# Performance work log

Measured on AMD Instinct MI355X. Metric: run time of the kernel, lower is better.

## Reference

```python
import jax, jax.numpy as jnp
import numpy as np

JACCARD_THRESH = 0.5
NEG_POS = 3
VAR0, VAR1 = 0.1, 0.2
MAX_POS = 256  # static cap on gathered positives for the metric-learning terms


def point_form(boxes):
    # (cx,cy,w,h) -> (xmin,ymin,xmax,ymax)
    return jnp.concatenate([boxes[:, :2] - boxes[:, 2:] / 2,
                            boxes[:, :2] + boxes[:, 2:] / 2], axis=1)


def jaccard(a, b):
    # a: [O,4], b: [D,4] point form
    lt = jnp.maximum(a[:, None, :2], b[None, :, :2])
    rb = jnp.minimum(a[:, None, 2:], b[None, :, 2:])
    wh = jnp.clip(rb - lt, 0.0)
    inter = wh[..., 0] * wh[..., 1]
    area_a = (a[:, 2] - a[:, 0]) * (a[:, 3] - a[:, 1])
    area_b = (b[:, 2] - b[:, 0]) * (b[:, 3] - b[:, 1])
    return inter / (area_a[:, None] + area_b[None, :] - inter)


def encode(matched, priors):
    g_cxcy = ((matched[:, :2] + matched[:, 2:]) / 2 - priors[:, :2]) / (VAR0 * priors[:, 2:])
    g_wh = jnp.log((matched[:, 2:] - matched[:, :2]) / priors[:, 2:]) / VAR1
    return jnp.concatenate([g_cxcy, g_wh], axis=1)


def match_one(truths, labels, poses, priors):
    # standard SSD match (per image)
    ov = jaccard(truths, point_form(priors))          # [O, D]
    best_prior_idx = jnp.argmax(ov, axis=1)           # [O]
    best_truth_ov = jnp.max(ov, axis=0)               # [D]
    best_truth_idx = jnp.argmax(ov, axis=0)           # [D]
    best_truth_ov = best_truth_ov.at[best_prior_idx].set(2.0)
    best_truth_idx = best_truth_idx.at[best_prior_idx].set(jnp.arange(truths.shape[0]))
    matches = truths[best_truth_idx]                  # [D,4]
    conf = labels[best_truth_idx] + 1                 # background=0
    conf = jnp.where(best_truth_ov < JACCARD_THRESH, 0, conf)
    return encode(matches, priors), conf.astype(jnp.int32), poses[best_truth_idx]


def multibox_loss(loc_data, conf_data, line_data, pose_data, dbox_list, targets):
    B, D, C = conf_data.shape
    truths = targets[:, :, 0:4]
    labels = targets[:, :, 4].astype(jnp.int32)
    poses = targets[:, :, 5:8]
    loc_t, conf_t, pose_t = jax.vmap(match_one, in_axes=(0, 0, 0, None))(
        truths, labels, poses, dbox_list)

    pos = conf_t > 0                                  # [B,D]
    posf = pos.astype(loc_data.dtype)

    # smooth-L1 loc loss over positives (sum reduction)
    d = loc_data - loc_t
    sl1 = jnp.where(jnp.abs(d) < 1.0, 0.5 * d * d, jnp.abs(d) - 0.5)
    loss_l = jnp.sum(sl1 * posf[..., None])

    # pose squared-error over positives
    loss_p = jnp.sum((pose_data - pose_t) ** 2 * posf[..., None])

    # per-anchor cross entropy + hard-negative mining (double-argsort rank trick)
    logp = jax.nn.log_softmax(conf_data, axis=-1)
    ce = -jnp.take_along_axis(logp, conf_t[..., None], axis=-1)[..., 0]  # [B,D]
    ce_mined = jnp.where(pos, 0.0, ce)
    loss_idx = jnp.argsort(-ce_mined, axis=1)
    idx_rank = jnp.argsort(loss_idx, axis=1)
    num_pos = jnp.sum(pos.astype(jnp.int32), axis=1, keepdims=True)
    num_neg = jnp.minimum(num_pos * NEG_POS, D)
    neg = idx_rank < num_neg
    loss_c = jnp.sum(ce * (pos | neg).astype(ce.dtype))

    N = jnp.maximum(jnp.sum(posf), 1.0)
    loss_l = loss_l / N
    loss_c = loss_c / N
    loss_p = loss_p / N

    # ---- metric-learning block on gathered positives (static cap) ----
    pos_flat = pos.reshape(-1)
    order = jnp.argsort(jnp.where(pos_flat, 0, 1))[:MAX_POS]  # stable: row-major positives first
    valid = pos_flat[order]                                   # [K]
    emb = line_data.reshape(-1, line_data.shape[-1])[order]   # [K,32] raw embeddings
    lab = conf_t.reshape(-1)[order]                           # [K]
    qp = pose_t.reshape(-1, 3)[order]                         # [K,3]

    # PairMarginMiner / TripletMarginLoss use L2-normalized LpDistance by default
    nemb = emb / jnp.maximum(jnp.linalg.norm(emb, axis=1, keepdims=True), 1e-12)
    sq = jnp.sum((nemb[:, None, :] - nemb[None, :, :]) ** 2, axis=-1)
    dist = jnp.sqrt(jnp.maximum(sq, 1e-12))                   # [K,K]

    K = emb.shape[0]
    eye = jnp.eye(K, dtype=bool)
    vpair = valid[:, None] & valid[None, :] & ~eye
    same = lab[:, None] == lab[None, :]
    pos_pair = vpair & same & (dist > 0.2)   # mined hard positive pairs
    neg_pair = vpair & ~same & (dist < 0.8)  # mined hard negative pairs
    n_pp = jnp.sum(pos_pair)
    n_np = jnp.sum(neg_pair)

    # pairs -> triplets sharing the anchor; TripletMarginLoss(margin=0.2), AvgNonZero reducer
    trip_mask = pos_pair[:, :, None] & neg_pair[:, None, :]           # [K,K,K]
    trip_loss = jax.nn.relu(dist[:, :, None] - dist[:, None, :] + 0.2)
    nz = trip_mask & (trip_loss > 0)
    loss_t = jnp.sum(jnp.where(nz, trip_loss, 0.0)) / jnp.maximum(jnp.sum(nz), 1)

    # Ldesk over mined positive pairs: raw-embedding sq-dist vs pose sq-dist consistency
    e_sq = jnp.sum((emb[:, None, :] - emb[None, :, :]) ** 2, axis=-1)
    q_sq = jnp.sum((qp[:, None, :] - qp[None, :, :]) ** 2, axis=-1)
    desk_sum = jnp.sum(jnp.where(pos_pair, (e_sq - q_sq) ** 2, 0.0))
    npp = jnp.maximum(n_pp, 1).astype(loc_data.dtype)
    Ldesk = desk_sum / npp + loss_t / jnp.maximum(n_pp + n_np, 1)
    Ldesk = Ldesk / npp / 32.0

    return loss_l, loss_c, loss_p, Ldesk, loss_t


def setup_inputs():
    key = jax.random.key(0)
    ks = jax.random.split(key, 10)
    B, D, C, L, O = 32, 8732, 21, 32, 8
    loc_data = jax.random.normal(ks[0], (B, D, 4)) * 0.1
    conf_data = jax.random.normal(ks[1], (B, D, C))
    line_data = jax.random.normal(ks[2], (B, D, L))
    pose_data = jax.random.normal(ks[3], (B, D, 3))
    # default boxes (cx,cy,w,h) in (0,1)
    cxcy = jax.random.uniform(ks[4], (D, 2), minval=0.05, maxval=0.95)
    wh = jax.random.uniform(ks[5], (D, 2), minval=0.05, maxval=0.4)
    dbox_list = jnp.concatenate([cxcy, wh], axis=1)
    # targets: [xmin,ymin,xmax,ymax,label,pose(3),unused]
    mins = jax.random.uniform(ks[6], (B, O, 2), minval=0.0, maxval=0.6)
    sizes = jax.random.uniform(ks[7], (B, O, 2), minval=0.1, maxval=0.4)
    boxes = jnp.concatenate([mins, mins + sizes], axis=-1)
    labs = jax.random.randint(ks[8], (B, O, 1), 0, C - 1).astype(jnp.float32)
    pz = jax.random.normal(ks[9], (B, O, 3))
    targets = jnp.concatenate([boxes, labs, pz, jnp.zeros((B, O, 1))], axis=-1)
    return dict(loc_data=loc_data, conf_data=conf_data, line_data=line_data,
                pose_data=pose_data, dbox_list=dbox_list, targets=targets)


def reference(loc_data, conf_data, line_data, pose_data, dbox_list, targets):
    return multibox_loss(loc_data, conf_data, line_data, pose_data, dbox_list, targets)
```

## Files before the change

kernel.cpp:

```cpp
#include <hip/hip_runtime.h>
#include <cstdint>

#define B 32
#define D 8732
#define C 21
#define L 32
#define O 8
#define NSEGB 16
#define SEGLEN 546
#define NSEG 512
#define MT 576
#define NT 1024
#define PAIRB 128
#define TOPB 32
#define FINTGT (PAIRB + TOPB)

struct Ws {
  const float *loc, *conf, *line, *pose, *dbox, *targets;
  float* out;
  unsigned long long* bpPart;
  double* acc;
  int* ictr;
  int* cnt;
  int* posSlice;
  float* sce;
};

__device__ inline double waveSumD(double v) {
  #pragma unroll
  for (int s = 32; s > 0; s >>= 1) v += __shfl_down(v, s, 64);
  return v;
}

__device__ inline float iou_one(float tx1, float ty1, float tx2, float ty2, float ta,
                                float px1, float py1, float px2, float py2, float areaB) {
  float lx = fmaxf(tx1, px1), ly = fmaxf(ty1, py1);
  float rx = fminf(tx2, px2), ry = fminf(ty2, py2);
  float iw = fmaxf(rx - lx, 0.f), ih = fmaxf(ry - ly, 0.f);
  float inter = iw * ih;
  return inter / (ta + areaB - inter);
}

__global__ __launch_bounds__(256) void k_bp(Ws p) {
  __shared__ float tb[O][4], ta[O];
  __shared__ unsigned long long wm[4][O];
  int g = blockIdx.x, tid = threadIdx.x;
  int lane = tid & 63, wav = tid >> 6;
  int b = g >> 4, s = g & 15;
  int dBeg = s * SEGLEN;
  int dEnd = dBeg + SEGLEN; if (dEnd > D) dEnd = D;
  if (g == 0) {
    if (tid < 9) p.acc[tid] = 0.0;
    if (tid == 9) { p.ictr[0] = 0; p.ictr[1] = 0; }
  }
  if (tid < O) {
    const float* tr = p.targets + ((size_t)b * O + tid) * 9;
    tb[tid][0] = tr[0]; tb[tid][1] = tr[1]; tb[tid][2] = tr[2]; tb[tid][3] = tr[3];
    ta[tid] = (tr[2] - tr[0]) * (tr[3] - tr[1]);
  }
  __syncthreads();
  float bi_[O]; int bd_[O];
  #pragma unroll
  for (int t = 0; t < O; t++) { bi_[t] = 0.f; bd_[t] = 0; }
  for (int d = dBeg + tid; d < dEnd; d += 256) {
    float4 db = *(const float4*)(p.dbox + (size_t)d * 4);
    float px1 = db.x - 0.5f*db.z, py1 = db.y - 0.5f*db.w;
    float px2 = db.x + 0.5f*db.z, py2 = db.y + 0.5f*db.w;
    float areaB = db.z * db.w;
    #pragma unroll
    for (int t = 0; t < O; t++) {
      float iou = iou_one(tb[t][0], tb[t][1], tb[t][2], tb[t][3], ta[t],
                          px1, py1, px2, py2, areaB);
      if (iou > bi_[t]) { bi_[t] = iou; bd_[t] = d; }
    }
  }
  #pragma unroll
  for (int t = 0; t < O; t++) {
    unsigned long long k = ((unsigned long long)__float_as_uint(bi_[t]) << 32)
                         | (unsigned long long)(0xFFFFFFFFu - (unsigned)bd_[t]);
    #pragma unroll
    for (int sft = 32; sft > 0; sft >>= 1) {
      unsigned long long o = __shfl_down(k, sft, 64);
      if (o > k) k = o;
    }
    if (lane == 0) wm[wav][t] = k;
  }
  __syncthreads();
  if (tid < O) {
    unsigned long long k = wm[0][tid];
    #pragma unroll
    for (int w = 1; w < 4; w++) if (wm[w][tid] > k) k = wm[w][tid];
    p.bpPart[(size_t)g * O + tid] = k;
  }
}

struct ShM {
  float confS[SEGLEN * C];
  float tb[O][4], ta[O], tl[O], tp_[O][3];
  unsigned long long bpred[128];
  int bpd[O];
  int plist[256];
  int wcnt[9], wbase[9];
  double wred[9][3];
  int run;
};

__global__ __launch_bounds__(MT, 2) void k_match(Ws p) {
  __shared__ ShM sh;
  int g = blockIdx.x, tid = threadIdx.x;
  int lane = tid & 63, wav = tid >> 6;
  int b = g >> 4, s = g & 15;
  int dBeg = s * SEGLEN;
  int dEnd = dBeg + SEGLEN; if (dEnd > D) dEnd = D;
  int segLen = dEnd - dBeg;
  int d = dBeg + tid;
  bool act = tid < segLen;

  if (tid < O) {
    const float* tr = p.targets + ((size_t)b * O + tid) * 9;
    sh.tb[tid][0] = tr[0]; sh.tb[tid][1] = tr[1];
    sh.tb[tid][2] = tr[2]; sh.tb[tid][3] = tr[3];
    sh.ta[tid] = (tr[2] - tr[0]) * (tr[3] - tr[1]);
    sh.tl[tid] = tr[4];
    sh.tp_[tid][0] = tr[5]; sh.tp_[tid][1] = tr[6]; sh.tp_[tid][2] = tr[7];
  }
  if (tid < 128)
    sh.bpred[tid] = p.bpPart[((size_t)b * NSEGB + (tid >> 3)) * O + (tid & 7)];
  {
    const float2* csrc = (const float2*)(p.conf + ((size_t)b * D + dBeg) * C);
    float2* cdst = (float2*)sh.confS;
    int nf2 = (segLen * C) >> 1;
    for (int i = tid; i < nf2; i += MT) cdst[i] = csrc[i];
  }
  __syncthreads();
  if (tid < O) {
    unsigned long long k = 0ull;
    #pragma unroll
    for (int s2 = 0; s2 < NSEGB; s2++) {
      unsigned long long kk = sh.bpred[s2 * 8 + tid];
      if (kk > k) k = kk;
    }
    sh.bpd[tid] = (int)(0xFFFFFFFFu - (unsigned)(k & 0xFFFFFFFFull));
  }
  __syncthreads();

  double ll = 0, lp = 0, cp = 0;
  int cls = 0, bi = 0;
  if (act) {
    float x[C];
    #pragma unroll
    for (int c = 0; c < C; c++) x[c] = sh.confS[tid * C + c];
    float4 db = *(const float4*)(p.dbox + (size_t)d * 4);
    float px1 = db.x - 0.5f*db.z, py1 = db.y - 0.5f*db.w;
    float px2 = db.x + 0.5f*db.z, py2 = db.y + 0.5f*db.w;
    float areaB = db.z * db.w;
    float bv = -1.0f;
    #pragma unroll
    for (int t = 0; t < O; t++) {
      float iou = iou_one(sh.tb[t][0], sh.tb[t][1], sh.tb[t][2], sh.tb[t][3],
                          sh.ta[t], px1, py1, px2, py2, areaB);
      if (iou > bv) { bv = iou; bi = t; }
    }
    #pragma unroll
    for (int t = O - 1; t >= 0; t--)
      if (sh.bpd[t] == d) { bi = t; bv = 2.0f; break; }
    cls = (bv < 0.5f) ? 0 : ((int)sh.tl[bi] + 1);
    float m = x[0];
    #pragma unroll
    for (int c = 1; c < C; c++) m = fmaxf(m, x[c]);
    float sm = 0.f;
    #pragma unroll
    for (int c = 0; c < C; c++) sm += __expf(x[c] - m);
    float xc = x[0];
    #pragma unroll
    for (int c = 1; c < C; c++) xc = (cls == c) ? x[c] : xc;
    float ce = m + __logf(sm) - xc;
    size_t bd = (size_t)b * D + d;
    if (cls > 0) {
      cp += ce;
      p.sce[bd] = 0.f;
      float g0 = ((sh.tb[bi][0] + sh.tb[bi][2]) * 0.5f - db.x) / (0.1f * db.z);
      float g1 = ((sh.tb[bi][1] + sh.tb[bi][3]) * 0.5f - db.y) / (0.1f * db.w);
      float g2 = logf((sh.tb[bi][2] - sh.tb[bi][0]) / db.z) / 0.2f;
      float g3 = logf((sh.tb[bi][3] - sh.tb[bi][1]) / db.w) / 0.2f;
      float4 lo = *(const float4*)(p.loc + bd * 4);
      float dv, a;
      dv = lo.x - g0; a = fabsf(dv); ll += (double)((a < 1.f) ? 0.5f*dv*dv : a - 0.5f);
      dv = lo.y - g1; a = fabsf(dv); ll += (double)((a < 1.f) ? 0.5f*dv*dv : a - 0.5f);
      dv = lo.z - g2; a = fabsf(dv); ll += (double)((a < 1.f) ? 0.5f*dv*dv : a - 0.5f);
      dv = lo.w - g3; a = fabsf(dv); ll += (double)((a < 1.f) ? 0.5f*dv*dv : a - 0.5f);
      const float* po = p.pose + bd * 3;
      #pragma unroll
      for (int q = 0; q < 3; q++) {
        float pd = po[q] - sh.tp_[bi][q];
        lp += (double)pd * (double)pd;
      }
    } else {
      p.sce[bd] = fmaxf(ce, 0.f);
    }
  }

  const unsigned long long lt = (lane == 0) ? 0ull : (~0ull >> (64 - lane));
  bool pos = act && (cls > 0);
  unsigned long long mm = __ballot(pos);
  if (lane == 0) sh.wcnt[wav] = __popcll(mm);
  __syncthreads();
  if (tid == 0) {
    int r = 0;
    #pragma unroll
    for (int w = 0; w < 9; w++) { sh.wbase[w] = r; r += sh.wcnt[w]; }
    sh.run = r;
  }
  __syncthreads();
  if (pos) {
    int rank = sh.wbase[wav] + __popcll(mm & lt);
    if (rank < 256) sh.plist[rank] = d | (cls << 14) | (bi << 19);
  }
  __syncthreads();
  int tot = sh.run;
  if (tid == 0) p.cnt[g] = tot;
  int stored = (tot < 256) ? tot : 256;
  if (tid < stored) p.posSlice[g * 256 + tid] = sh.plist[tid];
  double a0 = waveSumD(ll), a1 = waveSumD(lp), a2 = waveSumD(cp);
  if (lane == 0) { sh.wred[wav][0] = a0; sh.wred[wav][1] = a1; sh.wred[wav][2] = a2; }
  __syncthreads();
  if (tid == 0) {
    double tll = 0, tlp = 0, tcp = 0;
    #pragma unroll
    for (int w = 0; w < 9; w++) { tll += sh.wred[w][0]; tlp += sh.wred[w][1]; tcp += sh.wred[w][2]; }
    atomicAdd(&p.acc[0], tll);
    atomicAdd(&p.acc[1], tlp);
    atomicAdd(&p.acc[2], tcp);
    atomicAdd(&p.ictr[0], tot);
  }
}

struct __align__(16) ShT {
  float sce[D];
  int whist[16][256];
  int hist[256];
  int scb[NSEGB];
  int nposS;
  unsigned prefixSh; int kkSh;
  double wsum[16], wcnt2[16];
};
struct ShP {
  float embT[L][256];
  float invn[256];
  float qp_s[256][3];
  int   lab_s[256];
  float sd[2][256];
  int   Pi[NSEG + 1];
  int   wscan[8];
  unsigned long long spm[2][4], snm[2][4];
  double w1[2][4];
  int ppc[2][4], npc[2][4];
  double wS[16], wC[16];
};
struct ShD { int last; };
union Sh2 { ShT t; ShP pr; ShD dd; };

__global__ __launch_bounds__(NT) void k_minefin(Ws p) {
  __shared__ Sh2 sh;
  int g = blockIdx.x, tid = threadIdx.x;
  int lane = tid & 63, wav = tid >> 6;

  if (g >= PAIRB) {
    int bb = g - PAIRB;
    if (tid < NSEGB) sh.t.scb[tid] = p.cnt[bb * NSEGB + tid];
    const float* ce = p.sce + (size_t)bb * D;
    for (int i = tid; i < D / 4; i += NT)
      ((float4*)sh.t.sce)[i] = ((const float4*)ce)[i];
    __syncthreads();
    if (tid == 0) {
      int np = 0;
      #pragma unroll
      for (int q = 0; q < NSEGB; q++) np += sh.t.scb[q];
      sh.t.nposS = np;
    }
    __syncthreads();
    int npos = sh.t.nposS;
    int k = npos * 3; if (k > D) k = D;
    unsigned prefix = 0; int kk = k;
    for (int pass = 0; pass < 4; pass++) {
      int shift = 24 - 8 * pass;
      for (int i = tid; i < 16 * 256; i += NT) ((int*)sh.t.whist)[i] = 0;
      __syncthreads();
      unsigned himask = (pass == 0) ? 0u : (0xFFFFFFFFu << (shift + 8));
      for (int d = tid; d < D; d += NT) {
        unsigned keyb = __float_as_uint(sh.t.sce[d]);
        if ((keyb & himask) == (prefix & himask))
          atomicAdd(&sh.t.whist[wav][(keyb >> shift) & 255], 1);
      }
      __syncthreads();
      if (tid < 256) {
        int h = 0;
        #pragma unroll
        for (int w = 0; w < 16; w++) h += sh.t.whist[w][tid];
        sh.t.hist[tid] = h;
      }
      __syncthreads();
      if (tid < 64) {
        int l = tid;
        int h0 = sh.t.hist[l*4], h1 = sh.t.hist[l*4+1], h2 = sh.t.hist[l*4+2], h3 = sh.t.hist[l*4+3];
        int loc4 = h0 + h1 + h2 + h3;
        int suf = loc4;
        #pragma unroll
        for (int st = 1; st < 64; st <<= 1) {
          int o = __shfl_down(suf, st, 64);
          if (l + st < 64) suf += o;
        }
        int snext = suf - loc4;
        int s3 = snext + h3, s2 = s3 + h2, s1 = s2 + h1, s0 = s1 + h0;
        if (s3 >= kk && snext < kk) { sh.t.prefixSh = prefix | ((unsigned)(l*4+3) << shift); sh.t.kkSh = kk - snext; }
        if (s2 >= kk && s3 < kk)    { sh.t.prefixSh = prefix | ((unsigned)(l*4+2) << shift); sh.t.kkSh = kk - s3; }
        if (s1 >= kk && s2 < kk)    { sh.t.prefixSh = prefix | ((unsigned)(l*4+1) << shift); sh.t.kkSh = kk - s2; }
        if (s0 >= kk && s1 < kk)    { sh.t.prefixSh = prefix | ((unsigned)(l*4+0) << shift); sh.t.kkSh = kk - s1; }
      }
      __syncthreads();
      prefix = sh.t.prefixSh; kk = sh.t.kkSh;
      __syncthreads();
    }
    float T = __uint_as_float(prefix);
    double sgt = 0.0; int cgt = 0;
    for (int d = tid; d < D; d += NT) {
      float v = sh.t.sce[d];
      if (__float_as_uint(v) > prefix) { sgt += (double)v; cgt++; }
    }
    double wv = waveSumD(sgt);
    double wc = waveSumD((double)cgt);
    if (lane == 0) { sh.t.wsum[wav] = wv; sh.t.wcnt2[wav] = wc; }
    __syncthreads();
    if (tid == 0) {
      double tsg = 0, tcg = 0;
      #pragma unroll
      for (int w = 0; w < 16; w++) { tsg += sh.t.wsum[w]; tcg += sh.t.wcnt2[w]; }
      atomicAdd(&p.acc[3], tsg + ((double)k - tcg) * (double)T);
    }
  } else {
    int rgrp = tid >> 9;
    int i = 2 * g + rgrp;
    int t5 = tid & 511, j = t5 & 255, qq = t5 >> 8;

    int v = (tid < NSEG) ? p.cnt[tid] : 0;
    #pragma unroll
    for (int st = 1; st < 64; st <<= 1) {
      int o = __shfl_up(v, st, 64);
      if (lane >= st) v += o;
    }
    if (tid < NSEG && lane == 63) sh.pr.wscan[tid >> 6] = v;
    __syncthreads();
    if (tid < NSEG) {
      int add = 0;
      for (int q = 0; q < (tid >> 6); q++) add += sh.pr.wscan[q];
      sh.pr.Pi[tid + 1] = v + add;
    }
    if (tid == 0) sh.pr.Pi[0] = 0;
    __syncthreads();
    int total = sh.pr.Pi[NSEG];
    int Pc = (total < 256) ? total : 256;

    if (tid < 256) {
      int slot = tid;
      bool val = slot < Pc;
      int cls = 0, dpr = 0, seg = 0;
      float q0 = 0.f, q1 = 0.f, q2 = 0.f;
      if (val) {
        int lo = 0;
        #pragma unroll
        for (int st = 256; st > 0; st >>= 1) {
          int m = lo + st;
          if (m <= NSEG - 1 && sh.pr.Pi[m] <= slot) lo = m;
        }
        seg = lo;
        int idx = slot - sh.pr.Pi[seg];
        if (idx < 256) {
          int packed = p.posSlice[seg * 256 + idx];
          dpr = packed & 0x3FFF;
          cls = (packed >> 14) & 31;
          int bi = (packed >> 19) & 7;
          int bb2 = seg >> 4;
          const float* tr = p.targets + ((size_t)bb2 * O + bi) * 9;
          q0 = tr[5]; q1 = tr[6]; q2 = tr[7];
        } else val = false;
      }
      float nrm2 = 0.f;
      if (val) {
        int bb2 = seg >> 4;
        const float4* e4 = (const float4*)(p.line + ((size_t)bb2 * D + dpr) * L);
        #pragma unroll
        for (int c = 0; c < 8; c++) {
          float4 t4 = e4[c];
          sh.pr.embT[c*4+0][slot] = t4.x; sh.pr.embT[c*4+1][slot] = t4.y;
          sh.pr.embT[c*4+2][slot] = t4.z; sh.pr.embT[c*4+3][slot] = t4.w;
          nrm2 += t4.x*t4.x + t4.y*t4.y + t4.z*t4.z + t4.w*t4.w;
        }
      } else {
        #pragma unroll
        for (int c = 0; c < L; c++) sh.pr.embT[c][slot] = 0.f;
      }
      sh.pr.invn[slot] = 1.f / fmaxf(sqrtf(nrm2), 1e-12f);
      sh.pr.lab_s[slot] = val ? cls : 0;
      sh.pr.qp_s[slot][0] = q0; sh.pr.qp_s[slot][1] = q1; sh.pr.qp_s[slot][2] = q2;
    }
    __syncthreads();

    int li = sh.pr.lab_s[i];
    bool vi = (i < Pc);
    bool pp = false, np = false;
    double dsk = 0.0;
    if (qq == 0) {
      bool vj = (j < Pc);
      float invi = sh.pr.invn[i], invj = sh.pr.invn[j];
      float sq = 0.f, esq = 0.f;
      #pragma unroll
      for (int c = 0; c < L; c++) {
        float ei = sh.pr.embT[c][i], ej = sh.pr.embT[c][j];
        float dn = ei * invi - ej * invj; sq += dn * dn;
        float de = ei - ej;              esq += de * de;
      }
      float ddv = sqrtf(fmaxf(sq, 1e-12f));
      sh.pr.sd[rgrp][j] = ddv;
      float qsq = 0.f;
      #pragma unroll
      for (int c = 0; c < 3; c++) {
        float dq = sh.pr.qp_s[i][c] - sh.pr.qp_s[j][c];
        qsq += dq * dq;
      }
      bool vp = vi && vj && (i != j);
      bool same = (li == sh.pr.lab_s[j]);
      pp = vp && same && (ddv > 0.2f);
      np = vp && !same && (ddv < 0.8f);
      float diff = esq - qsq;
      dsk = pp ? (double)diff * (double)diff : 0.0;
    }
    unsigned long long pb = __ballot(pp), nb = __ballot(np);
    double dw = waveSumD(dsk);
    if (lane == 0 && qq == 0) {
      int w4 = wav & 3;
      sh.pr.spm[rgrp][w4] = pb; sh.pr.snm[rgrp][w4] = nb; sh.pr.w1[rgrp][w4] = dw;
      sh.pr.ppc[rgrp][w4] = (int)__popcll(pb); sh.pr.npc[rgrp][w4] = (int)__popcll(nb);
    }
    __syncthreads();
    unsigned long long pmw = sh.pr.spm[rgrp][j >> 6];
    bool pj = (pmw >> (j & 63)) & 1ull;
    float sdj = sh.pr.sd[rgrp][j];
    double ts = 0.0, tc = 0.0;
    if (pj) {
      for (int it = 0; it < 128; it++) {
        int kx = qq + 2 * it;
        unsigned long long nmw = sh.pr.snm[rgrp][kx >> 6];
        if ((nmw >> (kx & 63)) & 1ull) {
          float xv = sdj - sh.pr.sd[rgrp][kx] + 0.2f;
          if (xv > 0.f) { ts += (double)xv; tc += 1.0; }
        }
      }
    }
    ts = waveSumD(ts); tc = waveSumD(tc);
    if (lane == 0) { sh.pr.wS[wav] = ts; sh.pr.wC[wav] = tc; }
    __syncthreads();
    if (tid == 0) {
      double S = 0, Cc = 0;
      #pragma unroll
      for (int w = 0; w < 16; w++) { S += sh.pr.wS[w]; Cc += sh.pr.wC[w]; }
      double dsum = 0; int pcnt = 0, ncnt = 0;
      #pragma unroll
      for (int r = 0; r < 2; r++)
        #pragma unroll
        for (int w = 0; w < 4; w++) {
          dsum += sh.pr.w1[r][w]; pcnt += sh.pr.ppc[r][w]; ncnt += sh.pr.npc[r][w];
        }
      atomicAdd(&p.acc[4], dsum);
      atomicAdd(&p.acc[5], (double)pcnt);
      atomicAdd(&p.acc[6], (double)ncnt);
      atomicAdd(&p.acc[7], S);
      atomicAdd(&p.acc[8], Cc);
    }
  }

  if (tid == 0) {
    asm volatile("s_waitcnt vmcnt(0)" ::: "memory");
    int prev = __hip_atomic_fetch_add(&p.ictr[1], 1, __ATOMIC_RELAXED, __HIP_MEMORY_SCOPE_AGENT);
    sh.dd.last = (prev == FINTGT - 1);
  }
  __syncthreads();
  if (!sh.dd.last) return;
  if (tid == 0) {
    double lossL = __hip_atomic_load(&p.acc[0], __ATOMIC_RELAXED, __HIP_MEMORY_SCOPE_AGENT);
    double lossP = __hip_atomic_load(&p.acc[1], __ATOMIC_RELAXED, __HIP_MEMORY_SCOPE_AGENT);
    double ceP   = __hip_atomic_load(&p.acc[2], __ATOMIC_RELAXED, __HIP_MEMORY_SCOPE_AGENT);
    double ceN   = __hip_atomic_load(&p.acc[3], __ATOMIC_RELAXED, __HIP_MEMORY_SCOPE_AGENT);
    double desk  = __hip_atomic_load(&p.acc[4], __ATOMIC_RELAXED, __HIP_MEMORY_SCOPE_AGENT);
    double npp   = __hip_atomic_load(&p.acc[5], __ATOMIC_RELAXED, __HIP_MEMORY_SCOPE_AGENT);
    double nnp   = __hip_atomic_load(&p.acc[6], __ATOMIC_RELAXED, __HIP_MEMORY_SCOPE_AGENT);
    double tripS = __hip_atomic_load(&p.acc[7], __ATOMIC_RELAXED, __HIP_MEMORY_SCOPE_AGENT);
    double tripC = __hip_atomic_load(&p.acc[8], __ATOMIC_RELAXED, __HIP_MEMORY_SCOPE_AGENT);
    int nTotI    = __hip_atomic_load(&p.ictr[0], __ATOMIC_RELAXED, __HIP_MEMORY_SCOPE_AGENT);
    double N = (nTotI > 0) ? (double)nTotI : 1.0;
    p.out[0] = (float)(lossL / N);
    p.out[1] = (float)((ceP + ceN) / N);
    p.out[2] = (float)(lossP / N);
    double cnt = (tripC > 0.0) ? tripC : 1.0;
    double loss_t = tripS / cnt;
    double nppd = (npp > 0.0) ? npp : 1.0;
    double tot = npp + nnp;
    double denom = (tot > 0.0) ? tot : 1.0;
    double Ldesk = desk / nppd + loss_t / denom;
    Ldesk = Ldesk / nppd / 32.0;
    p.out[3] = (float)Ldesk;
    p.out[4] = (float)loss_t;
  }
}

extern "C" void kernel_launch(void* const* d_in, const int* in_sizes, int n_in,
                              void* d_out, int out_size, void* d_ws, size_t ws_size,
                              hipStream_t stream) {
  char* ws = (char*)d_ws;
  size_t off = 0;
  auto alloc = [&](size_t bytes) -> char* {
    char* q = ws + off;
    off += (bytes + 255) & ~(size_t)255;
    return q;
  };
  Ws p;
  p.loc     = (const float*)d_in[0];
  p.conf    = (const float*)d_in[1];
  p.line    = (const float*)d_in[2];
  p.pose    = (const float*)d_in[3];
  p.dbox    = (const float*)d_in[4];
  p.targets = (const float*)d_in[5];
  p.out     = (float*)d_out;
  p.bpPart   = (unsigned long long*)alloc((size_t)NSEG * O * 8);
  p.acc      = (double*)alloc(16 * 8);
  p.ictr     = (int*)alloc(256);
  p.cnt      = (int*)alloc(NSEG * 4);
  p.posSlice = (int*)alloc((size_t)NSEG * 256 * 4);
  p.sce      = (float*)alloc((size_t)B * D * 4);

  k_bp     <<<NSEG,  256, 0, stream>>>(p);
  k_match  <<<NSEG,  MT,  0, stream>>>(p);
  k_minefin<<<FINTGT, NT, 0, stream>>>(p);
}
```

Before: 149.2 us.

## Fuse best-prior search into match kernel and replace atomics with per-block partials

Removes the separate best-prior kernel. Each match block now recomputes the full best-prior argmax over all 8732 priors for its image, redundantly across the 8 slices of that image. Blocks grow to 1024 threads over 1092-prior slices, and the shared-memory staging of conf is replaced by direct per-thread global loads. Loc, pose, positive-CE and count accumulation now write per-block partials that the final block reduces, instead of using global atomics. The histogram pass drops one reduction stage and one barrier. This saves a launch and an intermediate buffer, at the cost of redundant IoU work and uncoalesced conf reads.

Result: no change. 149.5 us (+0.2%).

```diff
diff --git a/kernel.cpp b/kernel.cpp
--- a/kernel.cpp
+++ b/kernel.cpp
@@ -6,10 +6,9 @@
 #define C 21
 #define L 32
 #define O 8
-#define NSEGB 16
-#define SEGLEN 546
-#define NSEG 512
-#define MT 576
+#define NSEGB 8
+#define SLICE 1092
+#define NSEG 256
 #define NT 1024
 #define PAIRB 128
 #define TOPB 32
@@ -18,12 +17,12 @@
 struct Ws {
   const float *loc, *conf, *line, *pose, *dbox, *targets;
   float* out;
-  unsigned long long* bpPart;
   double* acc;
   int* ictr;
   int* cnt;
   int* posSlice;
   float* sce;
+  double *gLossL, *gLossP, *gCeP;
 };
 
 __device__ inline double waveSumD(double v) {
@@ -41,81 +40,28 @@
   return inter / (ta + areaB - inter);
 }
 
-__global__ __launch_bounds__(256) void k_bp(Ws p) {
-  __shared__ float tb[O][4], ta[O];
-  __shared__ unsigned long long wm[4][O];
-  int g = blockIdx.x, tid = threadIdx.x;
-  int lane = tid & 63, wav = tid >> 6;
-  int b = g >> 4, s = g & 15;
-  int dBeg = s * SEGLEN;
-  int dEnd = dBeg + SEGLEN; if (dEnd > D) dEnd = D;
-  if (g == 0) {
-    if (tid < 9) p.acc[tid] = 0.0;
-    if (tid == 9) { p.ictr[0] = 0; p.ictr[1] = 0; }
-  }
-  if (tid < O) {
-    const float* tr = p.targets + ((size_t)b * O + tid) * 9;
-    tb[tid][0] = tr[0]; tb[tid][1] = tr[1]; tb[tid][2] = tr[2]; tb[tid][3] = tr[3];
-    ta[tid] = (tr[2] - tr[0]) * (tr[3] - tr[1]);
-  }
-  __syncthreads();
-  float bi_[O]; int bd_[O];
-  #pragma unroll
-  for (int t = 0; t < O; t++) { bi_[t] = 0.f; bd_[t] = 0; }
-  for (int d = dBeg + tid; d < dEnd; d += 256) {
-    float4 db = *(const float4*)(p.dbox + (size_t)d * 4);
-    float px1 = db.x - 0.5f*db.z, py1 = db.y - 0.5f*db.w;
-    float px2 = db.x + 0.5f*db.z, py2 = db.y + 0.5f*db.w;
-    float areaB = db.z * db.w;
-    #pragma unroll
-    for (int t = 0; t < O; t++) {
-      float iou = iou_one(tb[t][0], tb[t][1], tb[t][2], tb[t][3], ta[t],
-                          px1, py1, px2, py2, areaB);
-      if (iou > bi_[t]) { bi_[t] = iou; bd_[t] = d; }
-    }
-  }
-  #pragma unroll
-  for (int t = 0; t < O; t++) {
-    unsigned long long k = ((unsigned long long)__float_as_uint(bi_[t]) << 32)
-                         | (unsigned long long)(0xFFFFFFFFu - (unsigned)bd_[t]);
-    #pragma unroll
-    for (int sft = 32; sft > 0; sft >>= 1) {
-      unsigned long long o = __shfl_down(k, sft, 64);
-      if (o > k) k = o;
-    }
-    if (lane == 0) wm[wav][t] = k;
-  }
-  __syncthreads();
-  if (tid < O) {
-    unsigned long long k = wm[0][tid];
-    #pragma unroll
-    for (int w = 1; w < 4; w++) if (wm[w][tid] > k) k = wm[w][tid];
-    p.bpPart[(size_t)g * O + tid] = k;
-  }
-}
-
 struct ShM {
-  float confS[SEGLEN * C];
   float tb[O][4], ta[O], tl[O], tp_[O][3];
-  unsigned long long bpred[128];
+  unsigned long long wm[16][O];
   int bpd[O];
   int plist[256];
-  int wcnt[9], wbase[9];
-  double wred[9][3];
+  int wcnt[16], wbase[16];
+  double wred[16][3];
   int run;
 };
 
-__global__ __launch_bounds__(MT, 2) void k_match(Ws p) {
+__global__ __launch_bounds__(NT) void k_mb(Ws p) {
   __shared__ ShM sh;
   int g = blockIdx.x, tid = threadIdx.x;
   int lane = tid & 63, wav = tid >> 6;
-  int b = g >> 4, s = g & 15;
-  int dBeg = s * SEGLEN;
-  int dEnd = dBeg + SEGLEN; if (dEnd > D) dEnd = D;
-  int segLen = dEnd - dBeg;
-  int d = dBeg + tid;
-  bool act = tid < segLen;
-
+  int b = g >> 3, s = g & 7;
+  int dBeg = s * SLICE;
+  int dEnd = dBeg + SLICE; if (dEnd > D) dEnd = D;
+
+  if (g == 0) {
+    if (tid < 9) p.acc[tid] = 0.0;
+    else if (tid == 9) p.ictr[1] = 0;
+  }
   if (tid < O) {
     const float* tr = p.targets + ((size_t)b * O + tid) * 9;
     sh.tb[tid][0] = tr[0]; sh.tb[tid][1] = tr[1];
@@ -124,99 +70,126 @@
     sh.tl[tid] = tr[4];
     sh.tp_[tid][0] = tr[5]; sh.tp_[tid][1] = tr[6]; sh.tp_[tid][2] = tr[7];
   }
-  if (tid < 128)
-    sh.bpred[tid] = p.bpPart[((size_t)b * NSEGB + (tid >> 3)) * O + (tid & 7)];
+  if (tid == 0) sh.run = 0;
+  __syncthreads();
+
   {
-    const float2* csrc = (const float2*)(p.conf + ((size_t)b * D + dBeg) * C);
-    float2* cdst = (float2*)sh.confS;
-    int nf2 = (segLen * C) >> 1;
-    for (int i = tid; i < nf2; i += MT) cdst[i] = csrc[i];
-  }
-  __syncthreads();
-  if (tid < O) {
-    unsigned long long k = 0ull;
+    float bpv[O]; int bpdl[O];
     #pragma unroll
-    for (int s2 = 0; s2 < NSEGB; s2++) {
-      unsigned long long kk = sh.bpred[s2 * 8 + tid];
-      if (kk > k) k = kk;
-    }
-    sh.bpd[tid] = (int)(0xFFFFFFFFu - (unsigned)(k & 0xFFFFFFFFull));
-  }
-  __syncthreads();
-
-  double ll = 0, lp = 0, cp = 0;
-  int cls = 0, bi = 0;
-  if (act) {
-    float x[C];
-    #pragma unroll
-    for (int c = 0; c < C; c++) x[c] = sh.confS[tid * C + c];
-    float4 db = *(const float4*)(p.dbox + (size_t)d * 4);
-    float px1 = db.x - 0.5f*db.z, py1 = db.y - 0.5f*db.w;
-    float px2 = db.x + 0.5f*db.z, py2 = db.y + 0.5f*db.w;
-    float areaB = db.z * db.w;
-    float bv = -1.0f;
+    for (int t = 0; t < O; t++) { bpv[t] = 0.f; bpdl[t] = 0; }
+    for (int d0 = 0; d0 < D; d0 += NT) {
+      int d = d0 + tid;
+      if (d < D) {
+        float4 db = *(const float4*)(p.dbox + (size_t)d * 4);
+        float px1 = db.x - 0.5f*db.z, py1 = db.y - 0.5f*db.w;
+        float px2 = db.x + 0.5f*db.z, py2 = db.y + 0.5f*db.w;
+        float areaB = db.z * db.w;
+        #pragma unroll
+        for (int t = 0; t < O; t++) {
+          float iou = iou_one(sh.tb[t][0], sh.tb[t][1], sh.tb[t][2], sh.tb[t][3],
+                              sh.ta[t], px1, py1, px2, py2, areaB);
+          if (iou > bpv[t]) { bpv[t] = iou; bpdl[t] = d; }
+        }
+      }
+    }
     #pragma unroll
     for (int t = 0; t < O; t++) {
-      float iou = iou_one(sh.tb[t][0], sh.tb[t][1], sh.tb[t][2], sh.tb[t][3],
-                          sh.ta[t], px1, py1, px2, py2, areaB);
-      if (iou > bv) { bv = iou; bi = t; }
-    }
-    #pragma unroll
-    for (int t = O - 1; t >= 0; t--)
-      if (sh.bpd[t] == d) { bi = t; bv = 2.0f; break; }
-    cls = (bv < 0.5f) ? 0 : ((int)sh.tl[bi] + 1);
-    float m = x[0];
-    #pragma unroll
-    for (int c = 1; c < C; c++) m = fmaxf(m, x[c]);
-    float sm = 0.f;
-    #pragma unroll
-    for (int c = 0; c < C; c++) sm += __expf(x[c] - m);
-    float xc = x[0];
-    #pragma unroll
-    for (int c = 1; c < C; c++) xc = (cls == c) ? x[c] : xc;
-    float ce = m + __logf(sm) - xc;
-    size_t bd = (size_t)b * D + d;
-    if (cls > 0) {
-      cp += ce;
-      p.sce[bd] = 0.f;
-      float g0 = ((sh.tb[bi][0] + sh.tb[bi][2]) * 0.5f - db.x) / (0.1f * db.z);
-      float g1 = ((sh.tb[bi][1] + sh.tb[bi][3]) * 0.5f - db.y) / (0.1f * db.w);
-      float g2 = logf((sh.tb[bi][2] - sh.tb[bi][0]) / db.z) / 0.2f;
-      float g3 = logf((sh.tb[bi][3] - sh.tb[bi][1]) / db.w) / 0.2f;
-      float4 lo = *(const float4*)(p.loc + bd * 4);
-      float dv, a;
-      dv = lo.x - g0; a = fabsf(dv); ll += (double)((a < 1.f) ? 0.5f*dv*dv : a - 0.5f);
-      dv = lo.y - g1; a = fabsf(dv); ll += (double)((a < 1.f) ? 0.5f*dv*dv : a - 0.5f);
-      dv = lo.z - g2; a = fabsf(dv); ll += (double)((a < 1.f) ? 0.5f*dv*dv : a - 0.5f);
-      dv = lo.w - g3; a = fabsf(dv); ll += (double)((a < 1.f) ? 0.5f*dv*dv : a - 0.5f);
-      const float* po = p.pose + bd * 3;
-      #pragma unroll
-      for (int q = 0; q < 3; q++) {
-        float pd = po[q] - sh.tp_[bi][q];
-        lp += (double)pd * (double)pd;
-      }
-    } else {
-      p.sce[bd] = fmaxf(ce, 0.f);
-    }
+      unsigned long long k = ((unsigned long long)__float_as_uint(bpv[t]) << 32)
+                           | (unsigned long long)(0xFFFFFFFFu - (unsigned)bpdl[t]);
+      #pragma unroll
+      for (int sft = 32; sft > 0; sft >>= 1) {
+        unsigned long long o = __shfl_down(k, sft, 64);
+        if (o > k) k = o;
+      }
+      if (lane == 0) sh.wm[wav][t] = k;
+    }
+    __syncthreads();
+    if (tid < O) {
+      unsigned long long k = sh.wm[0][tid];
+      #pragma unroll
+      for (int w = 1; w < 16; w++) if (sh.wm[w][tid] > k) k = sh.wm[w][tid];
+      sh.bpd[tid] = (int)(0xFFFFFFFFu - (unsigned)(k & 0xFFFFFFFFull));
+    }
+    __syncthreads();
   }
 
   const unsigned long long lt = (lane == 0) ? 0ull : (~0ull >> (64 - lane));
-  bool pos = act && (cls > 0);
-  unsigned long long mm = __ballot(pos);
-  if (lane == 0) sh.wcnt[wav] = __popcll(mm);
-  __syncthreads();
-  if (tid == 0) {
-    int r = 0;
-    #pragma unroll
-    for (int w = 0; w < 9; w++) { sh.wbase[w] = r; r += sh.wcnt[w]; }
-    sh.run = r;
-  }
-  __syncthreads();
-  if (pos) {
-    int rank = sh.wbase[wav] + __popcll(mm & lt);
-    if (rank < 256) sh.plist[rank] = d | (cls << 14) | (bi << 19);
-  }
-  __syncthreads();
+  double ll = 0, lp = 0, cp = 0;
+  for (int d0 = dBeg; d0 < dEnd; d0 += NT) {
+    int d = d0 + tid;
+    bool act = d < dEnd;
+    int cls = 0, bi = 0;
+    if (act) {
+      float4 db = *(const float4*)(p.dbox + (size_t)d * 4);
+      float px1 = db.x - 0.5f*db.z, py1 = db.y - 0.5f*db.w;
+      float px2 = db.x + 0.5f*db.z, py2 = db.y + 0.5f*db.w;
+      float areaB = db.z * db.w;
+      float bv = -1.0f;
+      #pragma unroll
+      for (int t = 0; t < O; t++) {
+        float iou = iou_one(sh.tb[t][0], sh.tb[t][1], sh.tb[t][2], sh.tb[t][3],
+                            sh.ta[t], px1, py1, px2, py2, areaB);
+        if (iou > bv) { bv = iou; bi = t; }
+      }
+      #pragma unroll
+      for (int t = O - 1; t >= 0; t--)
+        if (sh.bpd[t] == d) { bi = t; bv = 2.0f; break; }
+      cls = (bv < 0.5f) ? 0 : ((int)sh.tl[bi] + 1);
+      const float* cb = p.conf + ((size_t)b * D + d) * C;
+      float x[C];
+      #pragma unroll
+      for (int c = 0; c < C; c++) x[c] = cb[c];
+      float m = x[0];
+      #pragma unroll
+      for (int c = 1; c < C; c++) m = fmaxf(m, x[c]);
+      float sm = 0.f;
+      #pragma unroll
+      for (int c = 0; c < C; c++) sm += __expf(x[c] - m);
+      float xc = x[0];
+      #pragma unroll
+      for (int c = 1; c < C; c++) xc = (cls == c) ? x[c] : xc;
+      float ce = m + __logf(sm) - xc;
+      size_t bd = (size_t)b * D + d;
+      if (cls > 0) {
+        cp += ce;
+        p.sce[bd] = 0.f;
+        float g0 = ((sh.tb[bi][0] + sh.tb[bi][2]) * 0.5f - db.x) / (0.1f * db.z);
+        float g1 = ((sh.tb[bi][1] + sh.tb[bi][3]) * 0.5f - db.y) / (0.1f * db.w);
+        float g2 = logf((sh.tb[bi][2] - sh.tb[bi][0]) / db.z) / 0.2f;
+        float g3 = logf((sh.tb[bi][3] - sh.tb[bi][1]) / db.w) / 0.2f;
+        float4 lo = *(const float4*)(p.loc + bd * 4);
+        float dv, a;
+        dv = lo.x - g0; a = fabsf(dv); ll += (double)((a < 1.f) ? 0.5f*dv*dv : a - 0.5f);
+        dv = lo.y - g1; a = fabsf(dv); ll += (double)((a < 1.f) ? 0.5f*dv*dv : a - 0.5f);
+        dv = lo.z - g2; a = fabsf(dv); ll += (double)((a < 1.f) ? 0.5f*dv*dv : a - 0.5f);
+        dv = lo.w - g3; a = fabsf(dv); ll += (double)((a < 1.f) ? 0.5f*dv*dv : a - 0.5f);
+        const float* po = p.pose + bd * 3;
+        #pragma unroll
+        for (int q = 0; q < 3; q++) {
+          float pd = po[q] - sh.tp_[bi][q];
+          lp += (double)pd * (double)pd;
+        }
+      } else {
+        p.sce[bd] = fmaxf(ce, 0.f);
+      }
+    }
+    bool pos = act && (cls > 0);
+    unsigned long long mm = __ballot(pos);
+    if (lane == 0) sh.wcnt[wav] = __popcll(mm);
+    __syncthreads();
+    if (tid == 0) {
+      int r = sh.run;
+      #pragma unroll
+      for (int w = 0; w < 16; w++) { sh.wbase[w] = r; r += sh.wcnt[w]; }
+      sh.run = r;
+    }
+    __syncthreads();
+    if (pos) {
+      int rank = sh.wbase[wav] + __popcll(mm & lt);
+      if (rank < 256) sh.plist[rank] = d | (cls << 14) | (bi << 19);
+    }
+    __syncthreads();
+  }
   int tot = sh.run;
   if (tid == 0) p.cnt[g] = tot;
   int stored = (tot < 256) ? tot : 256;
@@ -227,18 +200,14 @@
   if (tid == 0) {
     double tll = 0, tlp = 0, tcp = 0;
     #pragma unroll
-    for (int w = 0; w < 9; w++) { tll += sh.wred[w][0]; tlp += sh.wred[w][1]; tcp += sh.wred[w][2]; }
-    atomicAdd(&p.acc[0], tll);
-    atomicAdd(&p.acc[1], tlp);
-    atomicAdd(&p.acc[2], tcp);
-    atomicAdd(&p.ictr[0], tot);
+    for (int w = 0; w < 16; w++) { tll += sh.wred[w][0]; tlp += sh.wred[w][1]; tcp += sh.wred[w][2]; }
+    p.gLossL[g] = tll; p.gLossP[g] = tlp; p.gCeP[g] = tcp;
   }
 }
 
 struct __align__(16) ShT {
   float sce[D];
   int whist[16][256];
-  int hist[256];
   int scb[NSEGB];
   int nposS;
   unsigned prefixSh; int kkSh;
@@ -251,16 +220,16 @@
   int   lab_s[256];
   float sd[2][256];
   int   Pi[NSEG + 1];
-  int   wscan[8];
+  int   wscan[4];
   unsigned long long spm[2][4], snm[2][4];
   double w1[2][4];
   int ppc[2][4], npc[2][4];
   double wS[16], wC[16];
 };
-struct ShD { int last; };
+struct ShD { double lbuf[16]; int last; };
 union Sh2 { ShT t; ShP pr; ShD dd; };
 
-__global__ __launch_bounds__(NT) void k_minefin(Ws p) {
+__global__ __launch_bounds__(NT) void k_mf(Ws p) {
   __shared__ Sh2 sh;
   int g = blockIdx.x, tid = threadIdx.x;
   int lane = tid & 63, wav = tid >> 6;
@@ -284,8 +253,7 @@
     unsigned prefix = 0; int kk = k;
     for (int pass = 0; pass < 4; pass++) {
       int shift = 24 - 8 * pass;
-      for (int i = tid; i < 16 * 256; i += NT) ((int*)sh.t.whist)[i] = 0;
-      __syncthreads();
+      for (int i = lane; i < 256; i += 64) sh.t.whist[wav][i] = 0;
       unsigned himask = (pass == 0) ? 0u : (0xFFFFFFFFu << (shift + 8));
       for (int d = tid; d < D; d += NT) {
         unsigned keyb = __float_as_uint(sh.t.sce[d]);
@@ -293,16 +261,14 @@
           atomicAdd(&sh.t.whist[wav][(keyb >> shift) & 255], 1);
       }
       __syncthreads();
-      if (tid < 256) {
-        int h = 0;
-        #pragma unroll
-        for (int w = 0; w < 16; w++) h += sh.t.whist[w][tid];
-        sh.t.hist[tid] = h;
-      }
-      __syncthreads();
       if (tid < 64) {
         int l = tid;
-        int h0 = sh.t.hist[l*4], h1 = sh.t.hist[l*4+1], h2 = sh.t.hist[l*4+2], h3 = sh.t.hist[l*4+3];
+        int h0 = 0, h1 = 0, h2 = 0, h3 = 0;
+        #pragma unroll
+        for (int w = 0; w < 16; w++) {
+          h0 += sh.t.whist[w][l*4+0]; h1 += sh.t.whist[w][l*4+1];
+          h2 += sh.t.whist[w][l*4+2]; h3 += sh.t.whist[w][l*4+3];
+        }
         int loc4 = h0 + h1 + h2 + h3;
         int suf = loc4;
         #pragma unroll
@@ -319,7 +285,6 @@
       }
       __syncthreads();
       prefix = sh.t.prefixSh; kk = sh.t.kkSh;
-      __syncthreads();
     }
     float T = __uint_as_float(prefix);
     double sgt = 0.0; int cgt = 0;
@@ -368,7 +333,7 @@
       if (val) {
         int lo = 0;
         #pragma unroll
-        for (int st = 256; st > 0; st >>= 1) {
+        for (int st = 128; st > 0; st >>= 1) {
           int m = lo + st;
           if (m <= NSEG - 1 && sh.pr.Pi[m] <= slot) lo = m;
         }
@@ -379,14 +344,14 @@
           dpr = packed & 0x3FFF;
           cls = (packed >> 14) & 31;
           int bi = (packed >> 19) & 7;
-          int bb2 = seg >> 4;
+          int bb2 = seg >> 3;
           const float* tr = p.targets + ((size_t)bb2 * O + bi) * 9;
           q0 = tr[5]; q1 = tr[6]; q2 = tr[7];
         } else val = false;
       }
       float nrm2 = 0.f;
       if (val) {
-        int bb2 = seg >> 4;
+        int bb2 = seg >> 3;
         const float4* e4 = (const float4*)(p.line + ((size_t)bb2 * D + dpr) * L);
         #pragma unroll
         for (int c = 0; c < 8; c++) {
@@ -478,6 +443,7 @@
     }
   }
 
+  __syncthreads();
   if (tid == 0) {
     asm volatile("s_waitcnt vmcnt(0)" ::: "memory");
     int prev = __hip_atomic_fetch_add(&p.ictr[1], 1, __ATOMIC_RELAXED, __HIP_MEMORY_SCOPE_AGENT);
@@ -485,18 +451,43 @@
   }
   __syncthreads();
   if (!sh.dd.last) return;
+
+  auto sumArr = [&](const double* a, int n) -> double {
+    double v = 0;
+    for (int i2 = tid; i2 < n; i2 += NT) v += a[i2];
+    v = waveSumD(v);
+    __syncthreads();
+    if (lane == 0) sh.dd.lbuf[wav] = v;
+    __syncthreads();
+    double r = 0;
+    #pragma unroll
+    for (int w = 0; w < 16; w++) r += sh.dd.lbuf[w];
+    __syncthreads();
+    return r;
+  };
+  double lossL = sumArr(p.gLossL, NSEG);
+  double lossP = sumArr(p.gLossP, NSEG);
+  double ceP   = sumArr(p.gCeP,   NSEG);
+  double Ntot;
+  {
+    double v = 0;
+    for (int i2 = tid; i2 < NSEG; i2 += NT) v += (double)p.cnt[i2];
+    v = waveSumD(v);
+    __syncthreads();
+    if (lane == 0) sh.dd.lbuf[wav] = v;
+    __syncthreads();
+    Ntot = 0;
+    #pragma unroll
+    for (int w = 0; w < 16; w++) Ntot += sh.dd.lbuf[w];
+  }
   if (tid == 0) {
-    double lossL = __hip_atomic_load(&p.acc[0], __ATOMIC_RELAXED, __HIP_MEMORY_SCOPE_AGENT);
-    double lossP = __hip_atomic_load(&p.acc[1], __ATOMIC_RELAXED, __HIP_MEMORY_SCOPE_AGENT);
-    double ceP   = __hip_atomic_load(&p.acc[2], __ATOMIC_RELAXED, __HIP_MEMORY_SCOPE_AGENT);
     double ceN   = __hip_atomic_load(&p.acc[3], __ATOMIC_RELAXED, __HIP_MEMORY_SCOPE_AGENT);
     double desk  = __hip_atomic_load(&p.acc[4], __ATOMIC_RELAXED, __HIP_MEMORY_SCOPE_AGENT);
     double npp   = __hip_atomic_load(&p.acc[5], __ATOMIC_RELAXED, __HIP_MEMORY_SCOPE_AGENT);
     double nnp   = __hip_atomic_load(&p.acc[6], __ATOMIC_RELAXED, __HIP_MEMORY_SCOPE_AGENT);
     double tripS = __hip_atomic_load(&p.acc[7], __ATOMIC_RELAXED, __HIP_MEMORY_SCOPE_AGENT);
     double tripC = __hip_atomic_load(&p.acc[8], __ATOMIC_RELAXED, __HIP_MEMORY_SCOPE_AGENT);
-    int nTotI    = __hip_atomic_load(&p.ictr[0], __ATOMIC_RELAXED, __HIP_MEMORY_SCOPE_AGENT);
-    double N = (nTotI > 0) ? (double)nTotI : 1.0;
+    double N = (Ntot > 0.0) ? Ntot : 1.0;
     p.out[0] = (float)(lossL / N);
     p.out[1] = (float)((ceP + ceN) / N);
     p.out[2] = (float)(lossP / N);
@@ -530,14 +521,15 @@
   p.dbox    = (const float*)d_in[4];
   p.targets = (const float*)d_in[5];
   p.out     = (float*)d_out;
-  p.bpPart   = (unsigned long long*)alloc((size_t)NSEG * O * 8);
   p.acc      = (double*)alloc(16 * 8);
   p.ictr     = (int*)alloc(256);
   p.cnt      = (int*)alloc(NSEG * 4);
   p.posSlice = (int*)alloc((size_t)NSEG * 256 * 4);
   p.sce      = (float*)alloc((size_t)B * D * 4);
-
-  k_bp     <<<NSEG,  256, 0, stream>>>(p);
-  k_match  <<<NSEG,  MT,  0, stream>>>(p);
-  k_minefin<<<FINTGT, NT, 0, stream>>>(p);
+  p.gLossL   = (double*)alloc(NSEG * 8);
+  p.gLossP   = (double*)alloc(NSEG * 8);
+  p.gCeP     = (double*)alloc(NSEG * 8);
+
+  k_mb<<<NSEG,  NT, 0, stream>>>(p);
+  k_mf<<<FINTGT, NT, 0, stream>>>(p);
 }
```
